# Kernel tuning notes

Hardware: AMD Instinct MI355X
Metric: run time of the kernel (lower is better)

## Reference

```python
import jax, jax.numpy as jnp
import numpy as np

S = 3072        # packed sequence length
DIM = 1280      # hidden size
H = 16          # num heads
HD = DIM // H   # head dim = 80
NSEG = 3        # number of packed segments


def setup_inputs() -> dict:
    key = jax.random.key(0)
    ks = jax.random.split(key, 6)
    hidden_states = jax.random.normal(ks[0], (S, DIM), jnp.float32)
    cos = jax.random.uniform(ks[1], (S, HD), jnp.float32, minval=-1.0, maxval=1.0)
    sin = jax.random.uniform(ks[2], (S, HD), jnp.float32, minval=-1.0, maxval=1.0)
    qkv_w = jax.random.normal(ks[3], (3 * DIM, DIM), jnp.float32) * 0.02
    qkv_b = jnp.zeros((3 * DIM,), jnp.float32)
    proj_w = jax.random.normal(ks[4], (DIM, DIM), jnp.float32) * 0.02
    proj_b = jnp.zeros((DIM,), jnp.float32)
    # 3 equal segments; cu_seqlens = [0, 1024, 2048, 3072]
    cu_seqlens = jnp.arange(NSEG + 1, dtype=jnp.int32) * (S // NSEG)
    return {
        "hidden_states": hidden_states, "cos": cos, "sin": sin,
        "qkv_w": qkv_w, "qkv_b": qkv_b, "proj_w": proj_w, "proj_b": proj_b,
        "cu_seqlens": cu_seqlens,
    }


def rotate_half(x):
    x1, x2 = jnp.split(x, 2, axis=-1)
    return jnp.concatenate((-x2, x1), axis=-1)


def reference(hidden_states, cos, sin, qkv_w, qkv_b, proj_w, proj_b, cu_seqlens):
    seq = hidden_states.shape[0]
    # QKV projection: [S, 3*DIM] -> [S, 3, H, HD]
    qkv = (hidden_states @ qkv_w.T + qkv_b).reshape(seq, 3, H, HD)
    q, k, v = qkv[:, 0], qkv[:, 1], qkv[:, 2]  # each [S, H, HD]
    # RoPE in float32, cos/sin broadcast over heads via [S, 1, HD]
    c = cos[:, None, :].astype(jnp.float32)
    s = sin[:, None, :].astype(jnp.float32)
    qf, kf = q.astype(jnp.float32), k.astype(jnp.float32)
    q = (qf * c + rotate_half(qf) * s).astype(q.dtype)
    k = (kf * c + rotate_half(kf) * s).astype(k.dtype)
    # Block-diagonal additive mask from cu_seqlens (vectorized, no loop)
    pos = jnp.arange(seq)
    seg = jnp.searchsorted(cu_seqlens, pos, side="right")  # segment id per token
    neg = jnp.finfo(jnp.float32).min
    mask = jnp.where(seg[:, None] == seg[None, :], 0.0, neg)  # [S, S]
    # Dense attention over packed sequence
    scores = jnp.einsum("shd,thd->hst", q, k) / np.sqrt(HD).astype(np.float32)
    scores = scores + mask  # broadcast over heads
    attn = jax.nn.softmax(scores.astype(jnp.float32), axis=-1).astype(q.dtype)
    out = jnp.einsum("hst,thd->shd", attn, v).reshape(seq, DIM)
    return out @ proj_w.T + proj_b
```

## Files before the change

kernel.cpp:

```cpp
#include <hip/hip_runtime.h>
#include <hip/hip_bf16.h>


#define S_TOT 3072
#define DIM   1280
#define NH    16
#define HD    80
#define SEG   1024
#define TDIM  3840
#define K1    1280

typedef short v8s __attribute__((ext_vector_type(8)));
typedef float v4f __attribute__((ext_vector_type(4)));

__device__ __forceinline__ short f2bf(float v) {
  __hip_bfloat16 b = __float2bfloat16(v);
  return *reinterpret_cast<short*>(&b);
}

__device__ __forceinline__ float bf2f(short s) {
  unsigned u = ((unsigned)(unsigned short)s) << 16;
  float f;
  __builtin_memcpy(&f, &u, 4);
  return f;
}

__device__ __forceinline__ void gload16(const void* g, void* lds) {
  __builtin_amdgcn_global_load_lds(
      (const __attribute__((address_space(1))) char*)g,
      (__attribute__((address_space(3))) char*)lds, 16, 0, 0);
}

#define CVT_N1 (S_TOT * DIM / 4)
#define CVT_N2 (TDIM * DIM / 4)
#define CVT_N3 (DIM * DIM / 4)
__global__ __launch_bounds__(256) void cvt3(const float* __restrict__ in1,
                                            const float* __restrict__ in2,
                                            const float* __restrict__ in3,
                                            __hip_bfloat16* __restrict__ o1,
                                            __hip_bfloat16* __restrict__ o2,
                                            __hip_bfloat16* __restrict__ o3) {
  int i = blockIdx.x * 256 + threadIdx.x;
  const float* in;
  __hip_bfloat16* out;
  if (i < CVT_N1) { in = in1; out = o1; }
  else if (i < CVT_N1 + CVT_N2) { in = in2; out = o2; i -= CVT_N1; }
  else { in = in3; out = o3; i -= CVT_N1 + CVT_N2; }
  const float4 v = ((const float4*)in)[i];
  __hip_bfloat162 p0, p1;
  p0.x = __float2bfloat16(v.x); p0.y = __float2bfloat16(v.y);
  p1.x = __float2bfloat16(v.z); p1.y = __float2bfloat16(v.w);
  __hip_bfloat162* o = (__hip_bfloat162*)(out + (size_t)i * 4);
  o[0] = p0; o[1] = p1;
}

extern __shared__ short ring[];

__global__ __launch_bounds__(512, 2) void gemm1_3r(const __hip_bfloat16* __restrict__ A,
                                                   const __hip_bfloat16* __restrict__ B,
                                                   const float* __restrict__ bias,
                                                   __hip_bfloat16* __restrict__ C) {
  const int tid  = threadIdx.x;
  const int wave = tid >> 6;
  const int lane = tid & 63;
  const int quad = lane >> 4;
  const int l16  = lane & 15;
  const int wmp  = wave >> 2;
  const int wnp  = wave & 3;
  const int bm = blockIdx.x * 256;
  const int bn = blockIdx.y * 256;

  const int r0 = ((tid >> 3) << 1) + ((tid >> 2) & 1);
  const int gs = (tid & 3) ^ ((tid >> 3) & 3);
  const short* A0 = (const short*)A + (size_t)(bm + r0) * K1 + gs * 8;
  const short* A1 = A0 + (size_t)128 * K1;
  const short* B0 = (const short*)B + (size_t)(bn + r0) * K1 + gs * 8;
  const short* B1 = B0 + (size_t)128 * K1;
  const int wst = wave * 512;

#define STG(sbuf, ko) do {                              \
    short* d_ = ring + (sbuf) * 16384;                  \
    gload16(A0 + (ko), d_ + wst);                       \
    gload16(A1 + (ko), d_ + 4096 + wst);                \
    gload16(B0 + (ko), d_ + 8192 + wst);                \
    gload16(B1 + (ko), d_ + 12288 + wst);               \
  } while (0)

  const int posA  = quad ^ ((l16 >> 1) & 3);
  const int rbase = (l16 >> 1) * 64 + (l16 & 1) * 32 + posA * 8;
  const int Abase = wmp * 4096 + rbase;
  const int Bbase = 8192 + wnp * 2048 + rbase;

  v4f acc[8][4];
  const v4f vz = {0.f, 0.f, 0.f, 0.f};
  #pragma unroll
  for (int i = 0; i < 8; ++i)
    #pragma unroll
    for (int j = 0; j < 4; ++j) acc[i][j] = vz;

  STG(0, 0);
  STG(1, 32);
  asm volatile("s_waitcnt vmcnt(4)" ::: "memory");
  __builtin_amdgcn_s_barrier();
  __builtin_amdgcn_sched_barrier(0);

  int cb = 0, sb = 2;
  for (int t = 0; t < 40; ++t) {
    if (t + 2 < 40) STG(sb, (t + 2) * 32);

    const short* lb = ring + cb * 16384;
    v8s af[8], bf[4];
    #pragma unroll
    for (int i = 0; i < 8; ++i) af[i] = *(const v8s*)&lb[Abase + i * 512];
    #pragma unroll
    for (int j = 0; j < 4; ++j) bf[j] = *(const v8s*)&lb[Bbase + j * 512];

    __builtin_amdgcn_s_setprio(1);
    #pragma unroll
    for (int i = 0; i < 8; ++i)
      #pragma unroll
      for (int j = 0; j < 4; ++j)
        acc[i][j] = __builtin_amdgcn_mfma_f32_16x16x32_bf16(af[i], bf[j], acc[i][j], 0, 0, 0);
    __builtin_amdgcn_s_setprio(0);

    if (t < 39) {
      if (t + 2 < 40) asm volatile("s_waitcnt vmcnt(4)" ::: "memory");
      else            asm volatile("s_waitcnt vmcnt(0)" ::: "memory");
      __builtin_amdgcn_s_barrier();
      __builtin_amdgcn_sched_barrier(0);
    }
    cb = (cb == 2) ? 0 : cb + 1;
    sb = (sb == 2) ? 0 : sb + 1;
  }
#undef STG

  #pragma unroll
  for (int j = 0; j < 4; ++j) {
    const int col = bn + wnp * 64 + j * 16 + l16;
    const float bj = bias[col];
    #pragma unroll
    for (int i = 0; i < 8; ++i) {
      const int row0 = bm + wmp * 128 + i * 16 + quad * 4;
      #pragma unroll
      for (int r = 0; r < 4; ++r)
        C[(size_t)(row0 + r) * TDIM + col] = __float2bfloat16(acc[i][j][r] + bj);
    }
  }
}

__global__ __launch_bounds__(512, 2) void gemm2_3r(const __hip_bfloat16* __restrict__ A,
                                                   const __hip_bfloat16* __restrict__ B,
                                                   const float* __restrict__ bias,
                                                   float* __restrict__ C) {
  const int tid  = threadIdx.x;
  const int wave = tid >> 6;
  const int lane = tid & 63;
  const int quad = lane >> 4;
  const int l16  = lane & 15;
  const int wmp  = wave >> 2;
  const int wnp  = wave & 3;
  const int bm = blockIdx.x * 128;
  const int bn = blockIdx.y * 128;

  const int r0 = tid >> 3;
  const int p0 = tid & 7;
  const int gsw = p0 ^ (r0 & 7);
  const short* A0 = (const short*)A + (size_t)(bm + r0) * K1 + gsw * 8;
  const short* A1 = A0 + (size_t)64 * K1;
  const short* B0 = (const short*)B + (size_t)(bn + r0) * K1 + gsw * 8;
  const short* B1 = B0 + (size_t)64 * K1;
  const int wst = wave * 512;

#define STG2(sbuf, ko) do {                             \
    short* d_ = ring + (sbuf) * 16384;                  \
    gload16(A0 + (ko), d_ + wst);                       \
    gload16(A1 + (ko), d_ + 4096 + wst);                \
    gload16(B0 + (ko), d_ + 8192 + wst);                \
    gload16(B1 + (ko), d_ + 12288 + wst);               \
  } while (0)

  const int foff0 = l16 * 64 + ((quad) ^ (l16 & 7)) * 8;
  const int foff1 = l16 * 64 + ((4 + quad) ^ (l16 & 7)) * 8;
  const int Ab = wmp * 4096;
  const int Bb = 8192 + wnp * 2048;

  v4f acc[4][2];
  const v4f vz = {0.f, 0.f, 0.f, 0.f};
  #pragma unroll
  for (int i = 0; i < 4; ++i)
    #pragma unroll
    for (int j = 0; j < 2; ++j) acc[i][j] = vz;

  STG2(0, 0);
  STG2(1, 64);
  asm volatile("s_waitcnt vmcnt(4)" ::: "memory");
  __builtin_amdgcn_s_barrier();
  __builtin_amdgcn_sched_barrier(0);

  int cb = 0, sb = 2;
  for (int t = 0; t < 20; ++t) {
    if (t + 2 < 20) STG2(sb, (t + 2) * 64);

    const short* lb = ring + cb * 16384;
    #pragma unroll
    for (int s = 0; s < 2; ++s) {
      const int foff = s ? foff1 : foff0;
      v8s af[4], bf[2];
      #pragma unroll
      for (int i = 0; i < 4; ++i) af[i] = *(const v8s*)&lb[Ab + i * 1024 + foff];
      #pragma unroll
      for (int j = 0; j < 2; ++j) bf[j] = *(const v8s*)&lb[Bb + j * 1024 + foff];
      __builtin_amdgcn_s_setprio(1);
      #pragma unroll
      for (int i = 0; i < 4; ++i)
        #pragma unroll
        for (int j = 0; j < 2; ++j)
          acc[i][j] = __builtin_amdgcn_mfma_f32_16x16x32_bf16(af[i], bf[j], acc[i][j], 0, 0, 0);
      __builtin_amdgcn_s_setprio(0);
    }

    if (t < 19) {
      if (t + 2 < 20) asm volatile("s_waitcnt vmcnt(4)" ::: "memory");
      else            asm volatile("s_waitcnt vmcnt(0)" ::: "memory");
      __builtin_amdgcn_s_barrier();
      __builtin_amdgcn_sched_barrier(0);
    }
    cb = (cb == 2) ? 0 : cb + 1;
    sb = (sb == 2) ? 0 : sb + 1;
  }
#undef STG2

  #pragma unroll
  for (int j = 0; j < 2; ++j) {
    const int col = bn + wnp * 32 + j * 16 + l16;
    const float bj = bias[col];
    #pragma unroll
    for (int i = 0; i < 4; ++i) {
      const int row0 = bm + wmp * 64 + i * 16 + quad * 4;
      #pragma unroll
      for (int r = 0; r < 4; ++r)
        C[(size_t)(row0 + r) * DIM + col] = acc[i][j][r] + bj;
    }
  }
}

#define QK_BLOCKS ((2 * S_TOT * 16 * 12) / 256)
#define V_BLOCKS  ((3 * 16 * 16 * 8 * 96) / 256)
__global__ __launch_bounds__(256) void pack_all(const __hip_bfloat16* __restrict__ qkv,
                                                const float* __restrict__ cos_,
                                                const float* __restrict__ sin_,
                                                short* __restrict__ Qp,
                                                short* __restrict__ Kp,
                                                short* __restrict__ Vp) {
  const int bid = blockIdx.x;
  if (bid < QK_BLOCKS) {
    const int idx = bid * 256 + threadIdx.x;
    const int kd = idx % 12;
    const int h  = (idx / 12) % 16;
    const int s  = (idx / 192) % S_TOT;
    const int p  = idx / (192 * S_TOT);
    const int seg = s >> 10, tb = (s >> 6) & 15, t = s & 63;
    short* out = (p ? Kp : Qp) +
                 ((size_t)(((seg * 16 + h) * 16 + tb) * 12 + kd) * 64 + t) * 8;
    short tmp[8];
    if (kd >= 10) {
      #pragma unroll
      for (int j = 0; j < 8; ++j) tmp[j] = 0;
      *(int4*)out = *(int4*)tmp;
      return;
    }
    const short* row = (const short*)qkv + (size_t)s * TDIM + p * DIM + h * HD;
    const int d0 = kd * 8;
    const v8s xm = *(const v8s*)(row + d0);
    const v8s xr = *(const v8s*)(row + d0 + ((kd < 5) ? 40 : -40));
    const float sgn = (kd < 5) ? -1.f : 1.f;
    const float scale = (p == 0) ? 0.111803398874989485f : 1.0f;
    #pragma unroll
    for (int j = 0; j < 8; ++j) {
      const int d = d0 + j;
      const float v = (bf2f(xm[j]) * cos_[s * HD + d] +
                       sgn * bf2f(xr[j]) * sin_[s * HD + d]) * scale;
      tmp[j] = f2bf(v);
    }
    *(int4*)out = *(int4*)tmp;
  } else {
    const int idx = (bid - QK_BLOCKS) * 256 + threadIdx.x;
    const int d  = idx % 96;
    const int td = (idx / 96) % 8;
    const int tb = (idx / 768) % 16;
    const int h  = (idx / (768 * 16)) % 16;
    const int seg = idx / (768 * 256);
    const int s0 = seg * SEG + tb * 64 + td * 8;
    const short* q = (const short*)qkv;
    short tmp[8];
    if (d < 80) {
      #pragma unroll
      for (int j = 0; j < 8; ++j)
        tmp[j] = q[(size_t)(s0 + j) * TDIM + 2 * DIM + h * HD + d];
    } else {
      const short fill = (d == 80) ? (short)0x3F80 : (short)0;
      #pragma unroll
      for (int j = 0; j < 8; ++j) tmp[j] = fill;
    }
    *(int4*)(Vp + (size_t)idx * 8) = *(int4*)tmp;
  }
}

__global__ __launch_bounds__(256, 4) void attn_mfma(const short* __restrict__ Qp,
                                                    const short* __restrict__ Kp,
                                                    const short* __restrict__ Vp,
                                                    __hip_bfloat16* __restrict__ out) {
  __shared__ __align__(16) short Ks[64 * 96];
  __shared__ __align__(16) short Vs[64 * 96];
  __shared__ __align__(16) short Ps[4][16 * 68];

  const int l   = blockIdx.x;
  const int xcd = l & 7;
  const int j8  = l >> 3;
  const int g   = xcd * 6 + (j8 >> 4);
  const int qt  = j8 & 15;
  const int h   = g & 15;
  const int seg = g >> 4;
  const int tid  = threadIdx.x;
  const int wave = tid >> 6;
  const int lane = tid & 63;
  const int quad = lane >> 4;
  const int l16  = lane & 15;
  const int sh16 = g;

  const short* Qg = Qp + (size_t)(sh16 * 16 + qt) * 6144;
  const short* Kg = Kp + (size_t)sh16 * 16 * 6144;
  const short* Vg = Vp + (size_t)sh16 * 16 * 6144;

  v8s af[3];
  #pragma unroll
  for (int ks = 0; ks < 3; ++ks)
    af[ks] = *(const v8s*)(Qg + ((ks * 4 + quad) * 64 + wave * 16 + l16) * 8);

  v8s kr[3], vr[3];
  #pragma unroll
  for (int it = 0; it < 3; ++it) {
    const int o = (it * 256 + tid) * 8;
    kr[it] = *(const v8s*)(Kg + o);
    vr[it] = *(const v8s*)(Vg + o);
  }
  #pragma unroll
  for (int it = 0; it < 3; ++it) {
    const int o = (it * 256 + tid) * 8;
    *(v8s*)&Ks[o] = kr[it];
    *(v8s*)&Vs[o] = vr[it];
  }
  __syncthreads();

  v4f o4[6];
  const v4f vz = {0.f, 0.f, 0.f, 0.f};
  #pragma unroll
  for (int n = 0; n < 6; ++n) o4[n] = vz;

  for (int kb = 0; kb < 16; ++kb) {
    const bool more = (kb + 1 < 16);
    if (more) {
      const size_t base = (size_t)(kb + 1) * 6144;
      #pragma unroll
      for (int it = 0; it < 3; ++it) {
        const int o = (it * 256 + tid) * 8;
        kr[it] = *(const v8s*)(Kg + base + o);
        vr[it] = *(const v8s*)(Vg + base + o);
      }
    }

    v4f s4[4];
    #pragma unroll
    for (int j = 0; j < 4; ++j) {
      s4[j] = vz;
      #pragma unroll
      for (int ks = 0; ks < 3; ++ks) {
        const v8s bf = *(const v8s*)&Ks[((ks * 4 + quad) * 64 + j * 16 + l16) * 8];
        s4[j] = __builtin_amdgcn_mfma_f32_16x16x32_bf16(af[ks], bf, s4[j], 0, 0, 0);
      }
    }

    #pragma unroll
    for (int reg = 0; reg < 4; ++reg)
      #pragma unroll
      for (int j = 0; j < 4; ++j)
        Ps[wave][(quad * 4 + reg) * 68 + j * 16 + l16] = f2bf(__expf(s4[j][reg]));

    v8s pa[2];
    #pragma unroll
    for (int kp = 0; kp < 2; ++kp)
      pa[kp] = *(const v8s*)&Ps[wave][l16 * 68 + kp * 32 + quad * 8];
    #pragma unroll
    for (int n = 0; n < 6; ++n) {
      #pragma unroll
      for (int kp = 0; kp < 2; ++kp) {
        const v8s vb = *(const v8s*)&Vs[((kp * 4 + quad) * 96 + n * 16 + l16) * 8];
        o4[n] = __builtin_amdgcn_mfma_f32_16x16x32_bf16(pa[kp], vb, o4[n], 0, 0, 0);
      }
    }

    __syncthreads();
    if (more) {
      #pragma unroll
      for (int it = 0; it < 3; ++it) {
        const int o = (it * 256 + tid) * 8;
        *(v8s*)&Ks[o] = kr[it];
        *(v8s*)&Vs[o] = vr[it];
      }
    }
    __syncthreads();
  }

  float inv[4];
  #pragma unroll
  for (int r = 0; r < 4; ++r)
    inv[r] = 1.f / __shfl(o4[5][r], quad << 4);
  const int row0 = seg * SEG + qt * 64 + wave * 16 + quad * 4;
  #pragma unroll
  for (int n = 0; n < 5; ++n) {
    const int col = h * HD + n * 16 + l16;
    #pragma unroll
    for (int r = 0; r < 4; ++r)
      out[(size_t)(row0 + r) * DIM + col] = __float2bfloat16(o4[n][r] * inv[r]);
  }
}

extern "C" void kernel_launch(void* const* d_in, const int* in_sizes, int n_in,
                              void* d_out, int out_size, void* d_ws, size_t ws_size,
                              hipStream_t stream) {
  (void)in_sizes; (void)n_in; (void)out_size; (void)ws_size;
  const float* hs     = (const float*)d_in[0];
  const float* cosp   = (const float*)d_in[1];
  const float* sinp   = (const float*)d_in[2];
  const float* qkv_w  = (const float*)d_in[3];
  const float* qkv_b  = (const float*)d_in[4];
  const float* proj_w = (const float*)d_in[5];
  const float* proj_b = (const float*)d_in[6];

  float* out_f = (float*)d_out;
  __hip_bfloat16* qkv_b16 = (__hip_bfloat16*)d_ws;
  __hip_bfloat16* hs_b    = qkv_b16 + (size_t)S_TOT * TDIM;
  __hip_bfloat16* qkvw_b  = hs_b + (size_t)S_TOT * DIM;
  __hip_bfloat16* projw_b = qkvw_b + (size_t)TDIM * DIM;
  short* Qp = (short*)qkvw_b;
  short* Kp = (short*)(projw_b + (size_t)DIM * DIM);
  short* Vp = Kp + (size_t)3 * 16 * 16 * 6144;
  __hip_bfloat16* attn_b = hs_b;

  static bool attr_set = false;
  if (!attr_set) {
    hipFuncSetAttribute((const void*)gemm1_3r,
                        hipFuncAttributeMaxDynamicSharedMemorySize, 98304);
    hipFuncSetAttribute((const void*)gemm2_3r,
                        hipFuncAttributeMaxDynamicSharedMemorySize, 98304);
    attr_set = true;
  }

  cvt3<<<(CVT_N1 + CVT_N2 + CVT_N3) / 256, 256, 0, stream>>>(
      hs, qkv_w, proj_w, hs_b, qkvw_b, projw_b);

  gemm1_3r<<<dim3(S_TOT / 256, TDIM / 256), 512, 98304, stream>>>(
      hs_b, qkvw_b, qkv_b, qkv_b16);

  pack_all<<<QK_BLOCKS + V_BLOCKS, 256, 0, stream>>>(qkv_b16, cosp, sinp, Qp, Kp, Vp);

  attn_mfma<<<dim3(768), 256, 0, stream>>>(Qp, Kp, Vp, attn_b);

  gemm2_3r<<<dim3(S_TOT / 128, DIM / 128), 512, 98304, stream>>>(
      attn_b, projw_b, proj_b, out_f);
}
```

Before: 200.4 us.

## Switch QKV GEMM to double-buffered K=64 stages with 8-way LDS swizzle

Replaces the triple-buffered K=32 LDS ring in the QKV projection GEMM with a double-buffered ring of K=64 stages (64KB each, 128KB total), halving the number of barriers per K loop. The LDS layout and swizzle change to 64-element rows with an XOR over 8 chunks, and each stage issues two MFMA sub-steps. Launch bounds drop to one block per CU, so occupancy and latency hiding between blocks are reduced. Each stage also now waits for all outstanding loads before its barrier.

```diff
diff --git a/kernel.cpp b/kernel.cpp
--- a/kernel.cpp
+++ b/kernel.cpp
@@ -56,7 +56,7 @@
 
 extern __shared__ short ring[];
 
-__global__ __launch_bounds__(512, 2) void gemm1_3r(const __hip_bfloat16* __restrict__ A,
+__global__ __launch_bounds__(512, 1) void gemm1_2r(const __hip_bfloat16* __restrict__ A,
                                                    const __hip_bfloat16* __restrict__ B,
                                                    const float* __restrict__ bias,
                                                    __hip_bfloat16* __restrict__ C) {
@@ -70,26 +70,29 @@
   const int bm = blockIdx.x * 256;
   const int bn = blockIdx.y * 256;
 
-  const int r0 = ((tid >> 3) << 1) + ((tid >> 2) & 1);
-  const int gs = (tid & 3) ^ ((tid >> 3) & 3);
-  const short* A0 = (const short*)A + (size_t)(bm + r0) * K1 + gs * 8;
-  const short* A1 = A0 + (size_t)128 * K1;
-  const short* B0 = (const short*)B + (size_t)(bn + r0) * K1 + gs * 8;
-  const short* B1 = B0 + (size_t)128 * K1;
+  const int r0  = tid >> 3;
+  const int p0  = tid & 7;
+  const int gsw = p0 ^ (r0 & 7);
+  const short* Ag = (const short*)A + (size_t)(bm + r0) * K1 + gsw * 8;
+  const short* Bg = (const short*)B + (size_t)(bn + r0) * K1 + gsw * 8;
   const int wst = wave * 512;
 
-#define STG(sbuf, ko) do {                              \
-    short* d_ = ring + (sbuf) * 16384;                  \
-    gload16(A0 + (ko), d_ + wst);                       \
-    gload16(A1 + (ko), d_ + 4096 + wst);                \
-    gload16(B0 + (ko), d_ + 8192 + wst);                \
-    gload16(B1 + (ko), d_ + 12288 + wst);               \
+#define STG(sbuf, ko) do {                                        \
+    short* d_ = ring + (sbuf) * 32768;                            \
+    gload16(Ag + (ko),                 d_ + wst);                 \
+    gload16(Ag + 64 * K1 + (ko),       d_ + 4096 + wst);          \
+    gload16(Ag + 128 * K1 + (ko),      d_ + 8192 + wst);          \
+    gload16(Ag + 192 * K1 + (ko),      d_ + 12288 + wst);         \
+    gload16(Bg + (ko),                 d_ + 16384 + wst);         \
+    gload16(Bg + 64 * K1 + (ko),       d_ + 16384 + 4096 + wst);  \
+    gload16(Bg + 128 * K1 + (ko),      d_ + 16384 + 8192 + wst);  \
+    gload16(Bg + 192 * K1 + (ko),      d_ + 16384 + 12288 + wst); \
   } while (0)
 
-  const int posA  = quad ^ ((l16 >> 1) & 3);
-  const int rbase = (l16 >> 1) * 64 + (l16 & 1) * 32 + posA * 8;
-  const int Abase = wmp * 4096 + rbase;
-  const int Bbase = 8192 + wnp * 2048 + rbase;
+  const int foff0 = l16 * 64 + ((quad) ^ (l16 & 7)) * 8;
+  const int foff1 = l16 * 64 + ((4 + quad) ^ (l16 & 7)) * 8;
+  const int Ab = wmp * 8192;
+  const int Bb = 16384 + wnp * 4096;
 
   v4f acc[8][4];
   const v4f vz = {0.f, 0.f, 0.f, 0.f};
@@ -99,38 +102,37 @@
     for (int j = 0; j < 4; ++j) acc[i][j] = vz;
 
   STG(0, 0);
-  STG(1, 32);
-  asm volatile("s_waitcnt vmcnt(4)" ::: "memory");
+  asm volatile("s_waitcnt vmcnt(0)" ::: "memory");
   __builtin_amdgcn_s_barrier();
   __builtin_amdgcn_sched_barrier(0);
 
-  int cb = 0, sb = 2;
-  for (int t = 0; t < 40; ++t) {
-    if (t + 2 < 40) STG(sb, (t + 2) * 32);
-
-    const short* lb = ring + cb * 16384;
-    v8s af[8], bf[4];
-    #pragma unroll
-    for (int i = 0; i < 8; ++i) af[i] = *(const v8s*)&lb[Abase + i * 512];
-    #pragma unroll
-    for (int j = 0; j < 4; ++j) bf[j] = *(const v8s*)&lb[Bbase + j * 512];
-
-    __builtin_amdgcn_s_setprio(1);
-    #pragma unroll
-    for (int i = 0; i < 8; ++i)
-      #pragma unroll
-      for (int j = 0; j < 4; ++j)
-        acc[i][j] = __builtin_amdgcn_mfma_f32_16x16x32_bf16(af[i], bf[j], acc[i][j], 0, 0, 0);
-    __builtin_amdgcn_s_setprio(0);
-
-    if (t < 39) {
-      if (t + 2 < 40) asm volatile("s_waitcnt vmcnt(4)" ::: "memory");
-      else            asm volatile("s_waitcnt vmcnt(0)" ::: "memory");
+  for (int t = 0; t < 20; ++t) {
+    const int cur = t & 1;
+    if (t + 1 < 20) STG(1 - cur, (t + 1) * 64);
+
+    const short* lb = ring + cur * 32768;
+    #pragma unroll
+    for (int s = 0; s < 2; ++s) {
+      const int foff = s ? foff1 : foff0;
+      v8s af[8], bf[4];
+      #pragma unroll
+      for (int i = 0; i < 8; ++i) af[i] = *(const v8s*)&lb[Ab + i * 1024 + foff];
+      #pragma unroll
+      for (int j = 0; j < 4; ++j) bf[j] = *(const v8s*)&lb[Bb + j * 1024 + foff];
+      __builtin_amdgcn_s_setprio(1);
+      #pragma unroll
+      for (int i = 0; i < 8; ++i)
+        #pragma unroll
+        for (int j = 0; j < 4; ++j)
+          acc[i][j] = __builtin_amdgcn_mfma_f32_16x16x32_bf16(af[i], bf[j], acc[i][j], 0, 0, 0);
+      __builtin_amdgcn_s_setprio(0);
+    }
+
+    if (t + 1 < 20) {
+      asm volatile("s_waitcnt vmcnt(0)" ::: "memory");
       __builtin_amdgcn_s_barrier();
       __builtin_amdgcn_sched_barrier(0);
     }
-    cb = (cb == 2) ? 0 : cb + 1;
-    sb = (sb == 2) ? 0 : sb + 1;
   }
 #undef STG
 
@@ -449,8 +451,8 @@
 
   static bool attr_set = false;
   if (!attr_set) {
-    hipFuncSetAttribute((const void*)gemm1_3r,
-                        hipFuncAttributeMaxDynamicSharedMemorySize, 98304);
+    hipFuncSetAttribute((const void*)gemm1_2r,
+                        hipFuncAttributeMaxDynamicSharedMemorySize, 131072);
     hipFuncSetAttribute((const void*)gemm2_3r,
                         hipFuncAttributeMaxDynamicSharedMemorySize, 98304);
     attr_set = true;
@@ -459,7 +461,7 @@
   cvt3<<<(CVT_N1 + CVT_N2 + CVT_N3) / 256, 256, 0, stream>>>(
       hs, qkv_w, proj_w, hs_b, qkvw_b, projw_b);
 
-  gemm1_3r<<<dim3(S_TOT / 256, TDIM / 256), 512, 98304, stream>>>(
+  gemm1_2r<<<dim3(S_TOT / 256, TDIM / 256), 512, 131072, stream>>>(
       hs_b, qkvw_b, qkv_b, qkv_b16);
 
   pack_all<<<QK_BLOCKS + V_BLOCKS, 256, 0, stream>>>(qkv_b16, cosp, sinp, Qp, Kp, Vp);
```

After: 201.2 us. About the same (+0.4%).
